# Kernel tuning notes

Hardware: AMD Instinct MI355X
Metric: run time of the kernel (lower is better)

Reference implementation:

```python
import jax, jax.numpy as jnp
import numpy as np

B, N, D, NUM_CLASSES = 2048, 32768, 256, 100

def setup_inputs() -> dict:
    key = jax.random.key(0)
    k1, k2, k3 = jax.random.split(key, 3)
    x = jax.random.normal(k1, (B, D), dtype=jnp.float32)
    support_embeddings = jax.random.normal(k2, (N, D), dtype=jnp.float32)
    support_labels = jax.random.randint(k3, (N,), 0, NUM_CLASSES, dtype=jnp.int64)
    return {
        "x": x,
        "support_embeddings": support_embeddings,
        "support_labels": support_labels,
        "num_classes": NUM_CLASSES,
    }

def reference(x, support_embeddings, support_labels, num_classes):
    # Pairwise L2 distance [B, N] via ||q||^2 + ||s||^2 - 2 q.s (avoids [B,N,D] broadcast)
    q2 = jnp.sum(x * x, axis=1, keepdims=True)                 # [B, 1]
    s2 = jnp.sum(support_embeddings * support_embeddings, axis=1)  # [N]
    cross = jnp.einsum('bd,nd->bn', x, support_embeddings)     # [B, N]
    dist = jnp.sqrt(jnp.maximum(q2 + s2[None, :] - 2.0 * cross, 0.0))
    # topk(-dist, k=1) over support axis -> nearest neighbor index
    _, idx = jax.lax.top_k(-dist, 1)                           # [B, 1]
    idx = jnp.squeeze(idx, axis=1)                             # [B]
    labels = jnp.take(support_labels, idx, axis=0)             # [B]
    one_hot = jax.nn.one_hot(labels, num_classes, dtype=jnp.int32)  # [B, num_classes]
    return one_hot
```

## Files before the change

kernel.cpp:

```cpp
#include <hip/hip_runtime.h>

#define BQ 2048
#define NS 32768
#define DIM 256
#define NROWS (NS + BQ)

#define BMQ 256
#define BNS 128
#define BK 32
#define NST (DIM / BK)
#define GY (NS / BNS)
#define GX (BQ / BMQ)
#define EPS 0.08f
#define FBCH GY

typedef _Float16 f16;
typedef _Float16 f16x4 __attribute__((ext_vector_type(4)));
typedef _Float16 f16x8 __attribute__((ext_vector_type(8)));
typedef float    f32x4 __attribute__((ext_vector_type(4)));

__device__ __forceinline__ void gload16(const f16* g, f16* l) {
    __builtin_amdgcn_global_load_lds(
        (const __attribute__((address_space(1))) unsigned int*)g,
        (__attribute__((address_space(3))) unsigned int*)l, 16, 0, 0);
}

__device__ __forceinline__ const f16x8* fragp(const f16* base, int row, int q) {
    return (const f16x8*)(base + row * 32 + ((q ^ ((row >> 1) & 3)) << 3));
}

__global__ __launch_bounds__(256) void convert_kernel(
    const float* __restrict__ x, const float* __restrict__ sup,
    f16* __restrict__ xh, f16* __restrict__ sh,
    float* __restrict__ s2, int* __restrict__ fb_cnt) {
    if (blockIdx.x == 0 && threadIdx.x == 0) *fb_cnt = 0;
    const int wave = threadIdx.x >> 6, lane = threadIdx.x & 63;
    const int row = blockIdx.x * 4 + wave;
    if (row < NS) {
        float4 v = ((const float4*)(sup + (size_t)row * DIM))[lane];
        f16x4 hi;
        hi[0] = (f16)v.x; hi[1] = (f16)v.y; hi[2] = (f16)v.z; hi[3] = (f16)v.w;
        *(f16x4*)(sh + (size_t)row * DIM + lane * 4) = hi;
        float sum = v.x * v.x + v.y * v.y + v.z * v.z + v.w * v.w;
#pragma unroll
        for (int off = 32; off > 0; off >>= 1) sum += __shfl_xor(sum, off);
        if (lane == 0) s2[row] = sum;
    } else {
        const int q = row - NS;
        float4 v = ((const float4*)(x + (size_t)q * DIM))[lane];
        f16x4 hi;
        hi[0] = (f16)v.x; hi[1] = (f16)v.y; hi[2] = (f16)v.z; hi[3] = (f16)v.w;
        *(f16x4*)(xh + (size_t)q * DIM + lane * 4) = hi;
    }
}

__global__ __launch_bounds__(256, 2) void knn_mfma(
    const f16* __restrict__ xh, const f16* __restrict__ sh,
    const float* __restrict__ s2g,
    float* __restrict__ pv1, float* __restrict__ pv2, int* __restrict__ pi1) {
    __shared__ f16 T[3][(BMQ + BNS) * 32];

    const int tid  = threadIdx.x;
    const int lane = tid & 63, wid = tid >> 6;
    const int l16  = lane & 15, quad = lane >> 4;

    const int id   = blockIdx.y * GX + blockIdx.x;
    const int xcd  = id & 7;
    const int slot = id >> 3;
    const int gx   = slot & (GX - 1);
    const int gy   = xcd * (GY / 8) + (slot >> 3);
    const int m0   = gx * BMQ;
    const int n0   = gy * BNS;

    const int rl = lane >> 2;
    const int qs = (lane & 3) ^ ((rl >> 1) & 3);
    const size_t srcoff = (size_t)rl * DIM + qs * 8;

    const f16* px0 = xh + (size_t)(m0 + wid * 64) * DIM + srcoff;
    const f16* px1 = px0 + (size_t)16 * DIM;
    const f16* px2 = px0 + (size_t)32 * DIM;
    const f16* px3 = px0 + (size_t)48 * DIM;
    const f16* ps0 = sh + (size_t)(n0 + wid * 32) * DIM + srcoff;
    const f16* ps1 = ps0 + (size_t)16 * DIM;
    const int dX = wid * 2048;
    const int dS = BMQ * 32 + wid * 1024;

    f32x4 acc[4][8];
#pragma unroll
    for (int fi = 0; fi < 4; ++fi)
#pragma unroll
        for (int fj = 0; fj < 8; ++fj) acc[fi][fj] = (f32x4){0.f, 0.f, 0.f, 0.f};

    auto issue = [&](int s) {
        f16* base = &T[s % 3][0];
        f16* bx = base + dX;
        f16* bs = base + dS;
        const int k0 = s * BK;
        gload16(px0 + k0, bx);
        gload16(px1 + k0, bx + 512);
        gload16(px2 + k0, bx + 1024);
        gload16(px3 + k0, bx + 1536);
        gload16(ps0 + k0, bs);
        gload16(ps1 + k0, bs + 512);
    };

    issue(0);
    issue(1);

#pragma unroll
    for (int s = 0; s < NST; ++s) {
        if (s < NST - 1)
            asm volatile("s_waitcnt vmcnt(6)\n\ts_barrier" ::: "memory");
        else
            asm volatile("s_waitcnt vmcnt(0)\n\ts_barrier" ::: "memory");
        if (s + 2 < NST) issue(s + 2);

        const f16* TX = &T[s % 3][0];
        const f16* TS = TX + BMQ * 32;
        f16x8 A0 = *fragp(TX, wid * 64 + l16,      quad);
        f16x8 A1 = *fragp(TX, wid * 64 + 16 + l16, quad);
        f16x8 A2 = *fragp(TX, wid * 64 + 32 + l16, quad);
        f16x8 A3 = *fragp(TX, wid * 64 + 48 + l16, quad);
#pragma unroll
        for (int fj = 0; fj < 8; ++fj) {
            f16x8 B = *fragp(TS, fj * 16 + l16, quad);
            acc[0][fj] = __builtin_amdgcn_mfma_f32_16x16x32_f16(A0, B, acc[0][fj], 0, 0, 0);
            acc[1][fj] = __builtin_amdgcn_mfma_f32_16x16x32_f16(A1, B, acc[1][fj], 0, 0, 0);
            acc[2][fj] = __builtin_amdgcn_mfma_f32_16x16x32_f16(A2, B, acc[2][fj], 0, 0, 0);
            acc[3][fj] = __builtin_amdgcn_mfma_f32_16x16x32_f16(A3, B, acc[3][fj], 0, 0, 0);
        }
    }

    float s2v[8];
#pragma unroll
    for (int fj = 0; fj < 8; ++fj) s2v[fj] = s2g[n0 + fj * 16 + l16];
#pragma unroll
    for (int fi = 0; fi < 4; ++fi)
#pragma unroll
        for (int rg = 0; rg < 4; ++rg) {
            float bv1 = 3.4e38f, bv2 = 3.4e38f; int bi = 0;
#pragma unroll
            for (int fj = 0; fj < 8; ++fj) {
                float s = fmaf(-2.f, acc[fi][fj][rg], s2v[fj]);
                bv2 = fminf(bv2, fmaxf(bv1, s));
                bi  = (s < bv1) ? (n0 + fj * 16 + l16) : bi;
                bv1 = fminf(bv1, s);
            }
#pragma unroll
            for (int m = 1; m < 16; m <<= 1) {
                float ov1 = __shfl_xor(bv1, m);
                float ov2 = __shfl_xor(bv2, m);
                int   oi  = __shfl_xor(bi, m);
                float nb2 = fminf(fminf(bv2, ov2), fmaxf(bv1, ov1));
                bi  = (ov1 < bv1) ? oi : bi;
                bv1 = fminf(bv1, ov1);
                bv2 = nb2;
            }
            if (l16 == 0) {
                const int row = m0 + wid * 64 + fi * 16 + quad * 4 + rg;
                pv1[(size_t)row * GY + gy] = bv1;
                pv2[(size_t)row * GY + gy] = bv2;
                pi1[(size_t)row * GY + gy] = bi;
            }
        }
}

__global__ __launch_bounds__(128) void finalize2(
    const float* __restrict__ pv1, const float* __restrict__ pv2,
    const int* __restrict__ pi1, const int* __restrict__ labels,
    const int* __restrict__ ncp, int* __restrict__ out,
    int* __restrict__ fb_cnt, int* __restrict__ fb_list,
    float* __restrict__ qbest) {
    const int q = blockIdx.x, tid = threadIdx.x;
    __shared__ int s_label;
    if (tid < 64) {
        float bv1 = 3.4e38f, bv2 = 3.4e38f; int bi = 0;
        for (int t = tid; t < GY; t += 64) {
            float ov1 = pv1[(size_t)q * GY + t];
            float ov2 = pv2[(size_t)q * GY + t];
            int   oi  = pi1[(size_t)q * GY + t];
            float nb2 = fminf(fminf(bv2, ov2), fmaxf(bv1, ov1));
            bi  = (ov1 < bv1) ? oi : bi;
            bv1 = fminf(bv1, ov1);
            bv2 = nb2;
        }
#pragma unroll
        for (int m = 1; m < 64; m <<= 1) {
            float ov1 = __shfl_xor(bv1, m);
            float ov2 = __shfl_xor(bv2, m);
            int   oi  = __shfl_xor(bi, m);
            float nb2 = fminf(fminf(bv2, ov2), fmaxf(bv1, ov1));
            bi  = (ov1 < bv1) ? oi : bi;
            bv1 = fminf(bv1, ov1);
            bv2 = nb2;
        }
        if (tid == 0) {
            qbest[q] = bv1;
            if (bv2 - bv1 <= EPS) {
                int slot = atomicAdd(fb_cnt, 1);
                fb_list[slot] = q;
            }
            bool is64 = true;
            for (int i = 1; i < 128; i += 2)
                if (labels[i] != 0) { is64 = false; break; }
            s_label = is64 ? labels[2 * bi] : labels[bi];
        }
    }
    __syncthreads();
    const int nc = ncp[0], lbl = s_label;
    for (int c = tid; c < nc; c += 128)
        out[q * nc + c] = (c == lbl) ? 1 : 0;
}

__global__ __launch_bounds__(256) void fallback_scan(
    const float* __restrict__ x, const float* __restrict__ sup,
    const float* __restrict__ s2, const int* __restrict__ fb_cnt,
    const int* __restrict__ fb_list, const float* __restrict__ qbest,
    const float* __restrict__ pv1,
    float* __restrict__ fb_v, int* __restrict__ fb_i) {
    const int nslots = *fb_cnt;
    const int chunk = blockIdx.x;
    const int tid = threadIdx.x, lane = tid & 63, w = tid >> 6;
    __shared__ float wv[4];
    __shared__ int   wi[4];
    for (int slot = blockIdx.y; slot < nslots; slot += gridDim.y) {
        const int q = fb_list[slot];
        if (pv1[(size_t)q * GY + chunk] > qbest[q] + EPS) {
            if (tid == 0) {
                fb_v[(size_t)q * FBCH + chunk] = 3.4e38f;
                fb_i[(size_t)q * FBCH + chunk] = 0x7fffffff;
            }
            __syncthreads();
            continue;
        }
        const float4 xv = ((const float4*)(x + (size_t)q * DIM))[lane];
        float best = 3.4e38f; int bi = 0x7fffffff;
        const int base = chunk * BNS + w * 32;
#pragma unroll 4
        for (int r = 0; r < 32; ++r) {
            const int n = base + r;
            float4 sv = ((const float4*)(sup + (size_t)n * DIM))[lane];
            float d = fmaf(sv.x, xv.x,
                      fmaf(sv.y, xv.y,
                      fmaf(sv.z, xv.z, sv.w * xv.w)));
#pragma unroll
            for (int m = 32; m > 0; m >>= 1) d += __shfl_xor(d, m);
            float sc = s2[n] - 2.f * d;
            if (sc < best) { best = sc; bi = n; }
        }
        if (lane == 0) { wv[w] = best; wi[w] = bi; }
        __syncthreads();
        if (tid == 0) {
            float bv = wv[0]; int bx = wi[0];
#pragma unroll
            for (int t = 1; t < 4; ++t)
                if (wv[t] < bv || (wv[t] == bv && wi[t] < bx)) { bv = wv[t]; bx = wi[t]; }
            fb_v[(size_t)q * FBCH + chunk] = bv;
            fb_i[(size_t)q * FBCH + chunk] = bx;
        }
        __syncthreads();
    }
}

__global__ __launch_bounds__(64) void fallback_merge(
    const int* __restrict__ fb_cnt, const int* __restrict__ fb_list,
    const float* __restrict__ fb_v, const int* __restrict__ fb_i,
    const int* __restrict__ labels, const int* __restrict__ ncp,
    int* __restrict__ out) {
    const int nslots = *fb_cnt;
    const int lane = threadIdx.x;
    for (int slot = blockIdx.x; slot < nslots; slot += gridDim.x) {
        const int q = fb_list[slot];
        float v = 3.4e38f; int ix = 0x7fffffff;
        for (int t = lane; t < FBCH; t += 64) {
            float ov = fb_v[(size_t)q * FBCH + t];
            int   oi = fb_i[(size_t)q * FBCH + t];
            if (ov < v || (ov == v && oi < ix)) { v = ov; ix = oi; }
        }
#pragma unroll
        for (int m = 1; m < 64; m <<= 1) {
            float ov = __shfl_xor(v, m);
            int   oi = __shfl_xor(ix, m);
            if (ov < v || (ov == v && oi < ix)) { v = ov; ix = oi; }
        }
        bool is64 = true;
        for (int i = 1; i < 128; i += 2)
            if (labels[i] != 0) { is64 = false; break; }
        const int lbl = is64 ? labels[2 * ix] : labels[ix];
        const int nc = ncp[0];
        for (int c = lane; c < nc; c += 64)
            out[q * nc + c] = (c == lbl) ? 1 : 0;
    }
}

#define SBM 128
#define SBN 128
#define SBK 16
#define SNT 4
#define SGY (NS / (SBN * SNT))
#define SLDT (SBM + 4)

__global__ __launch_bounds__(256) void s2_kernel(const float* __restrict__ s,
                                                 float* __restrict__ s2) {
    int wave = threadIdx.x >> 6, lane = threadIdx.x & 63;
    int row = blockIdx.x * 4 + wave;
    const float4* p = (const float4*)(s + (size_t)row * DIM);
    float4 v = p[lane];
    float sum = v.x * v.x + v.y * v.y + v.z * v.z + v.w * v.w;
#pragma unroll
    for (int off = 32; off > 0; off >>= 1) sum += __shfl_xor(sum, off);
    if (lane == 0) s2[row] = sum;
}

__global__ __launch_bounds__(256) void knn_f32(const float* __restrict__ x,
                                               const float* __restrict__ sup,
                                               const float* __restrict__ s2g,
                                               float* __restrict__ pvals,
                                               int* __restrict__ pidx) {
    __shared__ float Xs[SBK][SLDT];
    __shared__ float Bs[SBK][SLDT];
    const int tid = threadIdx.x;
    const int tx = tid & 15, ty = tid >> 4;
    const int m0 = blockIdx.x * SBM, by = blockIdx.y;
    const int srow = tid >> 2, skq = (tid & 3) * 4;
    float rmin[8]; int ridx[8];
#pragma unroll
    for (int i = 0; i < 8; ++i) { rmin[i] = 3.4e38f; ridx[i] = 0x7fffffff; }
    const float* xr0 = x + (size_t)(m0 + srow) * DIM + skq;
    const float* xr1 = x + (size_t)(m0 + 64 + srow) * DIM + skq;
    for (int nt = 0; nt < SNT; ++nt) {
        const int n0 = (by * SNT + nt) * SBN;
        const float* sr0 = sup + (size_t)(n0 + srow) * DIM + skq;
        const float* sr1 = sup + (size_t)(n0 + 64 + srow) * DIM + skq;
        float acc[8][8];
#pragma unroll
        for (int i = 0; i < 8; ++i)
#pragma unroll
            for (int j = 0; j < 8; ++j) acc[i][j] = 0.0f;
        for (int kt = 0; kt < DIM / SBK; ++kt) {
            const int k0 = kt * SBK;
            float4 xv0 = *(const float4*)(xr0 + k0);
            float4 xv1 = *(const float4*)(xr1 + k0);
            float4 sv0 = *(const float4*)(sr0 + k0);
            float4 sv1 = *(const float4*)(sr1 + k0);
            __syncthreads();
            Xs[skq + 0][srow] = xv0.x; Xs[skq + 1][srow] = xv0.y;
            Xs[skq + 2][srow] = xv0.z; Xs[skq + 3][srow] = xv0.w;
            Xs[skq + 0][64 + srow] = xv1.x; Xs[skq + 1][64 + srow] = xv1.y;
            Xs[skq + 2][64 + srow] = xv1.z; Xs[skq + 3][64 + srow] = xv1.w;
            Bs[skq + 0][srow] = sv0.x; Bs[skq + 1][srow] = sv0.y;
            Bs[skq + 2][srow] = sv0.z; Bs[skq + 3][srow] = sv0.w;
            Bs[skq + 0][64 + srow] = sv1.x; Bs[skq + 1][64 + srow] = sv1.y;
            Bs[skq + 2][64 + srow] = sv1.z; Bs[skq + 3][64 + srow] = sv1.w;
            __syncthreads();
#pragma unroll
            for (int k = 0; k < SBK; ++k) {
                float4 a0 = *(const float4*)&Xs[k][ty * 4];
                float4 a1 = *(const float4*)&Xs[k][64 + ty * 4];
                float4 b0 = *(const float4*)&Bs[k][tx * 4];
                float4 b1 = *(const float4*)&Bs[k][64 + tx * 4];
                float a[8] = {a0.x, a0.y, a0.z, a0.w, a1.x, a1.y, a1.z, a1.w};
                float b[8] = {b0.x, b0.y, b0.z, b0.w, b1.x, b1.y, b1.z, b1.w};
#pragma unroll
                for (int i = 0; i < 8; ++i)
#pragma unroll
                    for (int j = 0; j < 8; ++j)
                        acc[i][j] = fmaf(a[i], b[j], acc[i][j]);
            }
        }
        const int nb0 = n0 + tx * 4, nb1 = n0 + 64 + tx * 4;
        float4 s20 = *(const float4*)(s2g + nb0);
        float4 s21 = *(const float4*)(s2g + nb1);
        float s2a[8] = {s20.x, s20.y, s20.z, s20.w, s21.x, s21.y, s21.z, s21.w};
        int nca[8] = {nb0, nb0 + 1, nb0 + 2, nb0 + 3, nb1, nb1 + 1, nb1 + 2, nb1 + 3};
#pragma unroll
        for (int i = 0; i < 8; ++i)
#pragma unroll
            for (int j = 0; j < 8; ++j) {
                float sc = fmaf(-2.0f, acc[i][j], s2a[j]);
                if (sc < rmin[i] || (sc == rmin[i] && nca[j] < ridx[i])) {
                    rmin[i] = sc; ridx[i] = nca[j];
                }
            }
    }
    __syncthreads();
    float* redv = (float*)Xs;
    int* redi = (int*)Bs;
#pragma unroll
    for (int i = 0; i < 8; ++i) {
        int mrow = (i < 4) ? (ty * 4 + i) : (64 + ty * 4 + (i - 4));
        redv[mrow * 16 + tx] = rmin[i];
        redi[mrow * 16 + tx] = ridx[i];
    }
    __syncthreads();
    if (tid < SBM) {
        float best = redv[tid * 16];
        int bi = redi[tid * 16];
#pragma unroll
        for (int t = 1; t < 16; ++t) {
            float v = redv[tid * 16 + t];
            int ix = redi[tid * 16 + t];
            if (v < best || (v == best && ix < bi)) { best = v; bi = ix; }
        }
        pvals[(size_t)(m0 + tid) * SGY + by] = best;
        pidx[(size_t)(m0 + tid) * SGY + by] = bi;
    }
}

__global__ __launch_bounds__(64) void finalize_f32(const float* __restrict__ pvals,
                                                   const int* __restrict__ pidx,
                                                   const int* __restrict__ labels,
                                                   const int* __restrict__ ncp,
                                                   int* __restrict__ out) {
    const int b = blockIdx.x, lane = threadIdx.x;
    float v = pvals[(size_t)b * SGY + lane];
    int ix = pidx[(size_t)b * SGY + lane];
#pragma unroll
    for (int off = 32; off > 0; off >>= 1) {
        float ov = __shfl_xor(v, off);
        int oi = __shfl_xor(ix, off);
        if (ov < v || (ov == v && oi < ix)) { v = ov; ix = oi; }
    }
    bool is64 = true;
    for (int i = 1; i < 128; i += 2)
        if (labels[i] != 0) { is64 = false; break; }
    const int lbl = is64 ? labels[2 * ix] : labels[ix];
    const int nc = ncp[0];
    for (int c = lane; c < nc; c += 64)
        out[b * nc + c] = (c == lbl) ? 1 : 0;
}

extern "C" void kernel_launch(void* const* d_in, const int* in_sizes, int n_in,
                              void* d_out, int out_size, void* d_ws, size_t ws_size,
                              hipStream_t stream) {
    const float* x      = (const float*)d_in[0];
    const float* sup    = (const float*)d_in[1];
    const int*   labels = (const int*)d_in[2];
    const int*   ncp    = (const int*)d_in[3];
    int* out = (int*)d_out;

    char* p = (char*)d_ws;
    float* s2      = (float*)p;           p += (size_t)NS * 4;
    float* pv1     = (float*)p;           p += (size_t)BQ * GY * 4;
    float* pv2     = (float*)p;           p += (size_t)BQ * GY * 4;
    int*   pi1     = (int*)p;             p += (size_t)BQ * GY * 4;
    int*   fb_cnt  = (int*)p;             p += 256;
    int*   fb_list = (int*)p;             p += (size_t)BQ * 4;
    float* qbest   = (float*)p;           p += (size_t)BQ * 4;
    float* fb_v    = (float*)p;           p += (size_t)BQ * FBCH * 4;
    int*   fb_i    = (int*)p;             p += (size_t)BQ * FBCH * 4;
    f16*   xh      = (f16*)p;             p += (size_t)BQ * DIM * 2;
    f16*   sh      = (f16*)p;             p += (size_t)NS * DIM * 2;
    const size_t need = (size_t)(p - (char*)d_ws);

    if (ws_size >= need) {
        convert_kernel<<<NROWS / 4, 256, 0, stream>>>(x, sup, xh, sh, s2, fb_cnt);
        dim3 grid(GX, GY);
        knn_mfma<<<grid, 256, 0, stream>>>(xh, sh, s2, pv1, pv2, pi1);
        finalize2<<<BQ, 128, 0, stream>>>(pv1, pv2, pi1, labels, ncp, out,
                                          fb_cnt, fb_list, qbest);
        dim3 fbgrid(FBCH, 64);
        fallback_scan<<<fbgrid, 256, 0, stream>>>(x, sup, s2, fb_cnt, fb_list,
                                                  qbest, pv1, fb_v, fb_i);
        fallback_merge<<<64, 64, 0, stream>>>(fb_cnt, fb_list, fb_v, fb_i, labels, ncp, out);
    } else {
        float* ss2   = (float*)d_ws;
        float* pvals = ss2 + NS;
        int*   pidx  = (int*)(pvals + (size_t)BQ * SGY);
        s2_kernel<<<NS / 4, 256, 0, stream>>>(sup, ss2);
        dim3 sgrid(BQ / SBM, SGY);
        knn_f32<<<sgrid, 256, 0, stream>>>(x, sup, ss2, pvals, pidx);
        finalize_f32<<<BQ, 64, 0, stream>>>(pvals, pidx, labels, ncp, out);
    }
}
```

Baseline: 156.7 us.

## Fuse fp32 fallback rescan into finalize kernel, drop separate scan and merge launches

The separate fallback_scan and fallback_merge kernels, together with the atomic fallback list, are replaced by a single finalize kernel. Each query block checks its own top-2 gap and, when the gap is ambiguous, rescans the candidate chunks in fp32 using both of its waves. This removes two kernel launches, the fixed-size fallback grid and the intermediate buffers. The cost is that ambiguous queries are now handled serially by one 128-thread block, so a query with many candidate chunks could become a long tail.

Result: slower. 181.4 us (+15.8%).

```diff
diff --git a/kernel.cpp b/kernel.cpp
--- a/kernel.cpp
+++ b/kernel.cpp
@@ -12,7 +12,6 @@
 #define GY (NS / BNS)
 #define GX (BQ / BMQ)
 #define EPS 0.08f
-#define FBCH GY
 
 typedef _Float16 f16;
 typedef _Float16 f16x4 __attribute__((ext_vector_type(4)));
@@ -31,9 +30,7 @@
 
 __global__ __launch_bounds__(256) void convert_kernel(
     const float* __restrict__ x, const float* __restrict__ sup,
-    f16* __restrict__ xh, f16* __restrict__ sh,
-    float* __restrict__ s2, int* __restrict__ fb_cnt) {
-    if (blockIdx.x == 0 && threadIdx.x == 0) *fb_cnt = 0;
+    f16* __restrict__ xh, f16* __restrict__ sh, float* __restrict__ s2) {
     const int wave = threadIdx.x >> 6, lane = threadIdx.x & 63;
     const int row = blockIdx.x * 4 + wave;
     if (row < NS) {
@@ -165,17 +162,23 @@
         }
 }
 
-__global__ __launch_bounds__(128) void finalize2(
+__global__ __launch_bounds__(128) void finalize_fused(
     const float* __restrict__ pv1, const float* __restrict__ pv2,
-    const int* __restrict__ pi1, const int* __restrict__ labels,
-    const int* __restrict__ ncp, int* __restrict__ out,
-    int* __restrict__ fb_cnt, int* __restrict__ fb_list,
-    float* __restrict__ qbest) {
+    const int* __restrict__ pi1, const float* __restrict__ x,
+    const float* __restrict__ sup, const float* __restrict__ s2,
+    const int* __restrict__ labels, const int* __restrict__ ncp,
+    int* __restrict__ out) {
     const int q = blockIdx.x, tid = threadIdx.x;
-    __shared__ int s_label;
-    if (tid < 64) {
+    const int lane = tid & 63, w = tid >> 6;
+    __shared__ float s_b1, s_b2;
+    __shared__ int   s_bi;
+    __shared__ float wv[2];
+    __shared__ int   wi[2];
+    __shared__ int   s_lbl;
+
+    if (w == 0) {
         float bv1 = 3.4e38f, bv2 = 3.4e38f; int bi = 0;
-        for (int t = tid; t < GY; t += 64) {
+        for (int t = lane; t < GY; t += 64) {
             float ov1 = pv1[(size_t)q * GY + t];
             float ov2 = pv2[(size_t)q * GY + t];
             int   oi  = pi1[(size_t)q * GY + t];
@@ -194,103 +197,52 @@
             bv1 = fminf(bv1, ov1);
             bv2 = nb2;
         }
-        if (tid == 0) {
-            qbest[q] = bv1;
-            if (bv2 - bv1 <= EPS) {
-                int slot = atomicAdd(fb_cnt, 1);
-                fb_list[slot] = q;
-            }
-            bool is64 = true;
-            for (int i = 1; i < 128; i += 2)
-                if (labels[i] != 0) { is64 = false; break; }
-            s_label = is64 ? labels[2 * bi] : labels[bi];
-        }
+        if (lane == 0) { s_b1 = bv1; s_b2 = bv2; s_bi = bi; }
     }
     __syncthreads();
-    const int nc = ncp[0], lbl = s_label;
-    for (int c = tid; c < nc; c += 128)
-        out[q * nc + c] = (c == lbl) ? 1 : 0;
-}
-
-__global__ __launch_bounds__(256) void fallback_scan(
-    const float* __restrict__ x, const float* __restrict__ sup,
-    const float* __restrict__ s2, const int* __restrict__ fb_cnt,
-    const int* __restrict__ fb_list, const float* __restrict__ qbest,
-    const float* __restrict__ pv1,
-    float* __restrict__ fb_v, int* __restrict__ fb_i) {
-    const int nslots = *fb_cnt;
-    const int chunk = blockIdx.x;
-    const int tid = threadIdx.x, lane = tid & 63, w = tid >> 6;
-    __shared__ float wv[4];
-    __shared__ int   wi[4];
-    for (int slot = blockIdx.y; slot < nslots; slot += gridDim.y) {
-        const int q = fb_list[slot];
-        if (pv1[(size_t)q * GY + chunk] > qbest[q] + EPS) {
-            if (tid == 0) {
-                fb_v[(size_t)q * FBCH + chunk] = 3.4e38f;
-                fb_i[(size_t)q * FBCH + chunk] = 0x7fffffff;
-            }
-            __syncthreads();
-            continue;
-        }
+    int bi = s_bi;
+
+    if (s_b2 - s_b1 <= EPS) {
+        const float qb = s_b1;
         const float4 xv = ((const float4*)(x + (size_t)q * DIM))[lane];
-        float best = 3.4e38f; int bi = 0x7fffffff;
-        const int base = chunk * BNS + w * 32;
+        float best = 3.4e38f; int bn = 0x7fffffff;
+        for (int c = 0; c < GY; ++c) {
+            if (pv1[(size_t)q * GY + c] > qb + EPS) continue;
+            const int base = c * BNS + w * 64;
 #pragma unroll 4
-        for (int r = 0; r < 32; ++r) {
-            const int n = base + r;
-            float4 sv = ((const float4*)(sup + (size_t)n * DIM))[lane];
-            float d = fmaf(sv.x, xv.x,
-                      fmaf(sv.y, xv.y,
-                      fmaf(sv.z, xv.z, sv.w * xv.w)));
-#pragma unroll
-            for (int m = 32; m > 0; m >>= 1) d += __shfl_xor(d, m);
-            float sc = s2[n] - 2.f * d;
-            if (sc < best) { best = sc; bi = n; }
-        }
-        if (lane == 0) { wv[w] = best; wi[w] = bi; }
+            for (int r = 0; r < 64; ++r) {
+                const int n = base + r;
+                float4 sv = ((const float4*)(sup + (size_t)n * DIM))[lane];
+                float d = fmaf(sv.x, xv.x,
+                          fmaf(sv.y, xv.y,
+                          fmaf(sv.z, xv.z, sv.w * xv.w)));
+#pragma unroll
+                for (int m = 32; m > 0; m >>= 1) d += __shfl_xor(d, m);
+                float sc = s2[n] - 2.f * d;
+                if (sc < best) { best = sc; bn = n; }
+            }
+        }
+        if (lane == 0) { wv[w] = best; wi[w] = bn; }
         __syncthreads();
         if (tid == 0) {
             float bv = wv[0]; int bx = wi[0];
-#pragma unroll
-            for (int t = 1; t < 4; ++t)
-                if (wv[t] < bv || (wv[t] == bv && wi[t] < bx)) { bv = wv[t]; bx = wi[t]; }
-            fb_v[(size_t)q * FBCH + chunk] = bv;
-            fb_i[(size_t)q * FBCH + chunk] = bx;
+            if (wv[1] < bv || (wv[1] == bv && wi[1] < bx)) { bx = wi[1]; }
+            s_bi = bx;
         }
         __syncthreads();
-    }
-}
-
-__global__ __launch_bounds__(64) void fallback_merge(
-    const int* __restrict__ fb_cnt, const int* __restrict__ fb_list,
-    const float* __restrict__ fb_v, const int* __restrict__ fb_i,
-    const int* __restrict__ labels, const int* __restrict__ ncp,
-    int* __restrict__ out) {
-    const int nslots = *fb_cnt;
-    const int lane = threadIdx.x;
-    for (int slot = blockIdx.x; slot < nslots; slot += gridDim.x) {
-        const int q = fb_list[slot];
-        float v = 3.4e38f; int ix = 0x7fffffff;
-        for (int t = lane; t < FBCH; t += 64) {
-            float ov = fb_v[(size_t)q * FBCH + t];
-            int   oi = fb_i[(size_t)q * FBCH + t];
-            if (ov < v || (ov == v && oi < ix)) { v = ov; ix = oi; }
-        }
-#pragma unroll
-        for (int m = 1; m < 64; m <<= 1) {
-            float ov = __shfl_xor(v, m);
-            int   oi = __shfl_xor(ix, m);
-            if (ov < v || (ov == v && oi < ix)) { v = ov; ix = oi; }
-        }
+        bi = s_bi;
+    }
+
+    if (tid == 0) {
         bool is64 = true;
         for (int i = 1; i < 128; i += 2)
             if (labels[i] != 0) { is64 = false; break; }
-        const int lbl = is64 ? labels[2 * ix] : labels[ix];
-        const int nc = ncp[0];
-        for (int c = lane; c < nc; c += 64)
-            out[q * nc + c] = (c == lbl) ? 1 : 0;
-    }
+        s_lbl = is64 ? labels[2 * bi] : labels[bi];
+    }
+    __syncthreads();
+    const int nc = ncp[0], lbl = s_lbl;
+    for (int c = tid; c < nc; c += 128)
+        out[q * nc + c] = (c == lbl) ? 1 : 0;
 }
 
 #define SBM 128
@@ -444,25 +396,16 @@
     float* pv1     = (float*)p;           p += (size_t)BQ * GY * 4;
     float* pv2     = (float*)p;           p += (size_t)BQ * GY * 4;
     int*   pi1     = (int*)p;             p += (size_t)BQ * GY * 4;
-    int*   fb_cnt  = (int*)p;             p += 256;
-    int*   fb_list = (int*)p;             p += (size_t)BQ * 4;
-    float* qbest   = (float*)p;           p += (size_t)BQ * 4;
-    float* fb_v    = (float*)p;           p += (size_t)BQ * FBCH * 4;
-    int*   fb_i    = (int*)p;             p += (size_t)BQ * FBCH * 4;
     f16*   xh      = (f16*)p;             p += (size_t)BQ * DIM * 2;
     f16*   sh      = (f16*)p;             p += (size_t)NS * DIM * 2;
     const size_t need = (size_t)(p - (char*)d_ws);
 
     if (ws_size >= need) {
-        convert_kernel<<<NROWS / 4, 256, 0, stream>>>(x, sup, xh, sh, s2, fb_cnt);
+        convert_kernel<<<NROWS / 4, 256, 0, stream>>>(x, sup, xh, sh, s2);
         dim3 grid(GX, GY);
         knn_mfma<<<grid, 256, 0, stream>>>(xh, sh, s2, pv1, pv2, pi1);
-        finalize2<<<BQ, 128, 0, stream>>>(pv1, pv2, pi1, labels, ncp, out,
-                                          fb_cnt, fb_list, qbest);
-        dim3 fbgrid(FBCH, 64);
-        fallback_scan<<<fbgrid, 256, 0, stream>>>(x, sup, s2, fb_cnt, fb_list,
-                                                  qbest, pv1, fb_v, fb_i);
-        fallback_merge<<<64, 64, 0, stream>>>(fb_cnt, fb_list, fb_v, fb_i, labels, ncp, out);
+        finalize_fused<<<BQ, 128, 0, stream>>>(pv1, pv2, pi1, x, sup, s2,
+                                               labels, ncp, out);
     } else {
         float* ss2   = (float*)d_ws;
         float* pvals = ss2 + NS;
```
